# Kernel tuning notes

Measured on AMD Instinct MI355X. Metric: run time of the kernel, lower is better.

Reference implementation:

```python
import jax, jax.numpy as jnp
import numpy as np

B, N, E = 4, 10000, 160000
F_EXOG = 8
IN_DIM = 9          # 1 (pm25) + F_EXOG
HIST, PRED = 8, 12
HID = 64
GNN_OUT = 13
E_HID, E_OUT = 32, 30
GRU_IN = IN_DIM + GNN_OUT  # 22


def setup_inputs() -> dict:
    key = jax.random.key(0)
    ks = jax.random.split(key, 16)
    s = 0.1
    return {
        "pm25_hist": jax.random.normal(ks[0], (B, HIST, N, 1), jnp.float32),
        "feature": jax.random.normal(ks[1], (B, HIST + PRED, N, F_EXOG), jnp.float32),
        "edge_attr": jax.random.uniform(ks[2], (E, 2), jnp.float32),
        "wind_mean": jnp.array([2.0, 180.0], jnp.float32),
        "wind_std": jnp.array([1.5, 90.0], jnp.float32),
        # edge MLP: Linear(21->32), Sigmoid, Linear(32->30), Sigmoid
        "e_w1": jax.random.normal(ks[3], (2 * IN_DIM + 3, E_HID), jnp.float32) * s,
        "e_b1": jnp.zeros((E_HID,), jnp.float32),
        "e_w2": jax.random.normal(ks[4], (E_HID, E_OUT), jnp.float32) * s,
        "e_b2": jnp.zeros((E_OUT,), jnp.float32),
        # node MLP: Linear(30->13), Sigmoid
        "n_w": jax.random.normal(ks[5], (E_OUT, GNN_OUT), jnp.float32) * s,
        "n_b": jnp.zeros((GNN_OUT,), jnp.float32),
        # GRUCell(22 -> 64), torch layout: weight_ih (3H, in), weight_hh (3H, H)
        "gru_wi": jax.random.normal(ks[6], (3 * HID, GRU_IN), jnp.float32) * s,
        "gru_wh": jax.random.normal(ks[7], (3 * HID, HID), jnp.float32) * s,
        "gru_bi": jnp.zeros((3 * HID,), jnp.float32),
        "gru_bh": jnp.zeros((3 * HID,), jnp.float32),
        # fc_out: Linear(64 -> 1)
        "fc_w": jax.random.normal(ks[8], (HID, 1), jnp.float32) * s,
        "fc_b": jnp.zeros((1,), jnp.float32),
        "edge_index": jax.random.randint(ks[9], (2, E), 0, N, jnp.int64),
    }


def _forward(pm25_hist, feature, edge_attr, wind_mean, wind_std,
             e_w1, e_b1, e_w2, e_b2, n_w, n_b,
             gru_wi, gru_wh, gru_bi, gru_bh, fc_w, fc_b, edge_index):
    batch, _, n_nodes, _ = pm25_hist.shape
    src, tgt = edge_index[0], edge_index[1]

    # buffers precomputed in __init__ (torch.std uses ddof=1)
    edge_mean = edge_attr.mean(axis=0, keepdims=True)
    edge_std = jnp.maximum(jnp.std(edge_attr, axis=0, ddof=1, keepdims=True), 1e-6)
    edge_attr_norm = (edge_attr - edge_mean) / edge_std          # (E, 2)
    city_dist = jnp.maximum(edge_attr[:, 0], 1e-3)               # (E,)
    city_direc = edge_attr[:, 1]                                 # (E,)
    w_std = jnp.maximum(wind_std, 1e-6)

    def graph_gnn(x):                                            # x: (B, N, IN_DIM)
        node_src = x[:, src]                                     # (B, E, IN_DIM)
        node_tgt = x[:, tgt]
        wind = node_src[..., -2:] * w_std + wind_mean            # de-normalize
        speed = jnp.maximum(wind[..., 0], 0.0)                   # (B, E)
        wdir = jnp.deg2rad(wind[..., 1])
        theta = jnp.abs(city_direc - wdir)
        edge_w = jax.nn.relu(3.0 * speed * jnp.cos(theta) / city_dist)  # (B, E)
        ean = jnp.broadcast_to(edge_attr_norm, (x.shape[0], E, 2))
        h = jnp.concatenate([node_src, node_tgt, ean, edge_w[..., None]], axis=-1)
        h = jax.nn.sigmoid(h @ e_w1 + e_b1)
        h = jax.nn.sigmoid(h @ e_w2 + e_b2)                      # (B, E, E_OUT)
        agg = jnp.zeros((x.shape[0], n_nodes, E_OUT), x.dtype)
        agg = agg.at[:, tgt].add(h).at[:, src].add(-h)           # scatter add / sub
        return jax.nn.sigmoid(agg @ n_w + n_b)                   # (B, N, GNN_OUT)

    def gru_step(h, x):                                          # h,x: (B*N, .)
        gi = x @ gru_wi.T + gru_bi
        gh = h @ gru_wh.T + gru_bh
        i_r, i_z, i_n = jnp.split(gi, 3, axis=-1)
        h_r, h_z, h_n = jnp.split(gh, 3, axis=-1)
        r = jax.nn.sigmoid(i_r + h_r)
        z = jax.nn.sigmoid(i_z + h_z)
        n = jnp.tanh(i_n + r * h_n)
        return (1.0 - z) * n + z * h

    def step(carry, feat_t):
        hn, xn = carry                                           # (B*N,HID), (B,N,1)
        x = jnp.concatenate([xn, feat_t], axis=-1)               # (B, N, IN_DIM)
        x_gnn = graph_gnn(x)
        xc = jnp.concatenate([x_gnn, x], axis=-1).reshape(batch * n_nodes, -1)
        hn = gru_step(hn, xc)
        xn = hn.reshape(batch, n_nodes, HID) @ fc_w + fc_b       # (B, N, 1)
        return (hn, xn), xn[..., 0]

    hn0 = jnp.zeros((batch * n_nodes, HID), pm25_hist.dtype)
    xn0 = pm25_hist[:, -1]                                       # (B, N, 1)
    feats = jnp.swapaxes(feature[:, HIST:HIST + PRED], 0, 1)     # (PRED, B, N, F)
    _, preds = jax.lax.scan(step, (hn0, xn0), feats)             # (PRED, B, N)
    return jnp.transpose(preds, (1, 2, 0))                       # (B, N, PRED)


def reference(pm25_hist, feature, edge_attr, wind_mean, wind_std,
              e_w1, e_b1, e_w2, e_b2, n_w, n_b,
              gru_wi, gru_wh, gru_bi, gru_bh, fc_w, fc_b, edge_index):
    return _forward(pm25_hist, feature, edge_attr, wind_mean, wind_std,
                    e_w1, e_b1, e_w2, e_b2, n_w, n_b,
                    gru_wi, gru_wh, gru_bi, gru_bh, fc_w, fc_b, edge_index)
```

## Files before the change

kernel.cpp:

```cpp
#include <hip/hip_runtime.h>
#include <hip/hip_fp16.h>
#include <cstddef>

#define BB    4
#define NN    10000
#define EE    160000
#define BN    40000
#define HISTC 8
#define PREDC 12
#define TSTEP 20
#define FEX   8
#define HIDC  64
#define EHID  32
#define EOUTC 30
#define GOUTC 13
#define GINC  22

typedef float v2f __attribute__((ext_vector_type(2)));
typedef _Float16 v2h __attribute__((ext_vector_type(2)));

struct alignas(16) WPack {
    __half2 w[16];
    float   nw[14];
    float   b2;
    float   pad;
};

__device__ __forceinline__ float fast_rcp(float x) { return __builtin_amdgcn_rcpf(x); }
__device__ __forceinline__ float sigm(float x) {
    return fast_rcp(1.0f + __expf(-x));
}
__device__ __forceinline__ v2f sigm2(v2f x) {
    v2f r; r.x = sigm(x.x); r.y = sigm(x.y); return r;
}
__device__ __forceinline__ float tanh_fast(float x) {
    x = fminf(fmaxf(x, -15.0f), 15.0f);
    float e = __expf(2.0f * x);
    return (e - 1.0f) * fast_rcp(e + 1.0f);
}

__device__ __forceinline__ float dot2(__half2 a, __half2 b, float c) {
#if __has_builtin(__builtin_amdgcn_fdot2)
    union { __half2 h; v2h v; } ua, ub;
    ua.h = a; ub.h = b;
    return __builtin_amdgcn_fdot2(ua.v, ub.v, c, false);
#else
    float2 fa = __half22float2(a), fb = __half22float2(b);
    return c + fa.x * fb.x + fa.y * fb.y;
#endif
}

__global__ __launch_bounds__(256) void stats1_kernel(const float* __restrict__ ea,
                                                     double* __restrict__ part) {
    __shared__ double sm[256][4];
    int tid = threadIdx.x;
    double s0 = 0, s1 = 0, q0 = 0, q1 = 0;
    for (int e = blockIdx.x * 256 + tid; e < EE; e += 256 * 256) {
        float2 v = reinterpret_cast<const float2*>(ea)[e];
        double v0 = (double)v.x, v1 = (double)v.y;
        s0 += v0; q0 += v0 * v0;
        s1 += v1; q1 += v1 * v1;
    }
    sm[tid][0] = s0; sm[tid][1] = s1; sm[tid][2] = q0; sm[tid][3] = q1;
    __syncthreads();
    for (int off = 128; off > 0; off >>= 1) {
        if (tid < off)
            for (int k = 0; k < 4; k++) sm[tid][k] += sm[tid + off][k];
        __syncthreads();
    }
    if (tid == 0) {
        part[blockIdx.x * 4 + 0] = sm[0][0];
        part[blockIdx.x * 4 + 1] = sm[0][1];
        part[blockIdx.x * 4 + 2] = sm[0][2];
        part[blockIdx.x * 4 + 3] = sm[0][3];
    }
}

__global__ __launch_bounds__(256) void stats2_kernel(const double* __restrict__ part,
                                                     float* __restrict__ stats) {
    __shared__ double sm[256][4];
    int tid = threadIdx.x;
    sm[tid][0] = part[tid * 4 + 0];
    sm[tid][1] = part[tid * 4 + 1];
    sm[tid][2] = part[tid * 4 + 2];
    sm[tid][3] = part[tid * 4 + 3];
    __syncthreads();
    for (int off = 128; off > 0; off >>= 1) {
        if (tid < off)
            for (int k = 0; k < 4; k++) sm[tid][k] += sm[tid + off][k];
        __syncthreads();
    }
    if (tid == 0) {
        double m0 = sm[0][0] / EE, m1 = sm[0][1] / EE;
        double v0 = (sm[0][2] - sm[0][0] * sm[0][0] / EE) / (double)(EE - 1);
        double v1 = (sm[0][3] - sm[0][1] * sm[0][1] / EE) / (double)(EE - 1);
        float sd0 = fmaxf((float)sqrt(v0 > 0 ? v0 : 0.0), 1e-6f);
        float sd1 = fmaxf((float)sqrt(v1 > 0 ? v1 : 0.0), 1e-6f);
        stats[0] = (float)m0; stats[1] = (float)m1;
        stats[2] = 1.0f / sd0; stats[3] = 1.0f / sd1;
    }
}

__global__ __launch_bounds__(256) void edgepre_kernel(
    const float* __restrict__ ea, const float* __restrict__ stats,
    float4* __restrict__ epre4)
{
    int e = blockIdx.x * 256 + threadIdx.x;
    if (e >= EE) return;
    float2 v = reinterpret_cast<const float2*>(ea)[e];
    float4 r;
    r.x = (v.x - stats[0]) * stats[2];
    r.y = (v.y - stats[1]) * stats[3];
    r.z = 1.0f / fmaxf(v.x, 1e-3f);
    r.w = v.y;
    epre4[e] = r;
}

__global__ __launch_bounds__(256) void cvtw_kernel(
    const float* __restrict__ wi, const float* __restrict__ wh,
    const float* __restrict__ ew2, const float* __restrict__ eb2,
    const float* __restrict__ nw,
    __half* __restrict__ wi_h, __half* __restrict__ wh_h,
    WPack* __restrict__ wpack)
{
    int i = blockIdx.x * 256 + threadIdx.x;
    if (i < 192 * GINC) wi_h[i] = __float2half(wi[i]);
    if (i < 192 * HIDC) wh_h[i] = __float2half(wh[i]);
    if (i < EOUTC) {
        WPack wp;
        #pragma unroll
        for (int q = 0; q < 16; q++)
            wp.w[q] = __floats2half2_rn(ew2[(2 * q) * EOUTC + i],
                                        ew2[(2 * q + 1) * EOUTC + i]);
        #pragma unroll
        for (int j = 0; j < GOUTC; j++) wp.nw[j] = nw[i * GOUTC + j];
        wp.nw[13] = 0.f;
        wp.b2 = eb2[i];
        wp.pad = 0.f;
        wpack[i] = wp;
    }
}

__global__ void initxn_kernel(const float* __restrict__ pm, float* __restrict__ xn) {
    int i = blockIdx.x * 256 + threadIdx.x;
    if (i >= BN) return;
    int b = i / NN, n = i - b * NN;
    xn[i] = pm[(b * HISTC + (HISTC - 1)) * NN + n];
}

__global__ void hist_kernel(const int* __restrict__ eidx,
                            int* __restrict__ deg_t, int* __restrict__ deg_s) {
    int e = blockIdx.x * 256 + threadIdx.x;
    if (e >= EE) return;
    atomicAdd(&deg_s[eidx[e]], 1);
    atomicAdd(&deg_t[eidx[EE + e]], 1);
}

__global__ __launch_bounds__(1024) void scan_kernel(
    const int* __restrict__ deg_t, const int* __restrict__ deg_s,
    int* __restrict__ off_t, int* __restrict__ off_s,
    int* __restrict__ cnt_t, int* __restrict__ cnt_s)
{
    __shared__ int pt[1024], ps[1024];
    int tid = threadIdx.x;
    int base = tid * 10;
    int st = 0, ss = 0;
    for (int k = 0; k < 10; k++) {
        int i = base + k;
        if (i < NN) { st += deg_t[i]; ss += deg_s[i]; }
    }
    pt[tid] = st; ps[tid] = ss;
    __syncthreads();
    for (int off = 1; off < 1024; off <<= 1) {
        int vt = (tid >= off) ? pt[tid - off] : 0;
        int vs = (tid >= off) ? ps[tid - off] : 0;
        __syncthreads();
        pt[tid] += vt; ps[tid] += vs;
        __syncthreads();
    }
    int ext = (tid == 0) ? 0 : pt[tid - 1];
    int exs = (tid == 0) ? 0 : ps[tid - 1];
    for (int k = 0; k < 10; k++) {
        int i = base + k;
        if (i < NN) {
            off_t[i] = ext; cnt_t[i] = ext;
            off_s[i] = exs; cnt_s[i] = exs;
            ext += deg_t[i]; exs += deg_s[i];
        }
    }
    if (tid == 0) { off_t[NN] = EE; off_s[NN] = EE; }
}

__global__ void fill_kernel(const int* __restrict__ eidx,
                            int* __restrict__ cnt_t, int* __restrict__ cnt_s,
                            int4* __restrict__ epos)
{
    int e = blockIdx.x * 256 + threadIdx.x;
    if (e >= EE) return;
    int s = eidx[e];
    int g = eidx[EE + e];
    int pt = atomicAdd(&cnt_t[g], 1);
    int ps = atomicAdd(&cnt_s[s], 1);
    int4 r; r.x = s; r.y = g; r.z = pt; r.w = ps;
    epos[e] = r;
}

__global__ void perm_kernel(const int4* __restrict__ epos,
                            const float4* __restrict__ epre4,
                            int4* __restrict__ eT, float4* __restrict__ epreT)
{
    int e = blockIdx.x * 256 + threadIdx.x;
    if (e >= EE) return;
    int4 p = epos[e];
    int slot = p.z;
    int4 r; r.x = p.x; r.y = p.y; r.z = p.w; r.w = 0;
    eT[slot] = r;
    epreT[slot] = epre4[e];
}

__global__ __launch_bounds__(256) void pre_kernel(
    float* __restrict__ xncur, const float* __restrict__ feature, int t,
    const float* __restrict__ xp,
    const float* __restrict__ fb,
    const float* __restrict__ ew1,
    const float* __restrict__ wmean, const float* __restrict__ wstd,
    __half* __restrict__ preS, __half* __restrict__ preT,
    float2* __restrict__ wind2, float* __restrict__ out)
{
    __shared__ alignas(16) float w1s[18 * EHID];
    for (int i = threadIdx.x; i < 18 * EHID; i += 256) w1s[i] = ew1[i];
    __syncthreads();
    int idx = blockIdx.x * 256 + threadIdx.x;
    if (idx >= BN * 8) return;
    int i = idx >> 3;
    int c = idx & 7;
    int b = i / NN, n = i - b * NN;
    float x0;
    if (t == 0) {
        x0 = xncur[i];
    } else {
        x0 = (xp[i] + xp[BN + i]) + (xp[2 * BN + i] + xp[3 * BN + i]) + fb[0];
        if (c == 0) {
            xncur[i] = x0;
            out[(size_t)i * PREDC + (t - 1)] = x0;
        }
    }
    float x[9];
    x[0] = x0;
    {
        const float4* fp = reinterpret_cast<const float4*>(
            feature + (((size_t)b * TSTEP + HISTC + t) * NN + n) * FEX);
        float4 u = fp[0], v = fp[1];
        x[1] = u.x; x[2] = u.y; x[3] = u.z; x[4] = u.w;
        x[5] = v.x; x[6] = v.y; x[7] = v.z; x[8] = v.w;
    }
    float4 aS = {0.f, 0.f, 0.f, 0.f}, aT = {0.f, 0.f, 0.f, 0.f};
    #pragma unroll
    for (int k = 0; k < 9; k++) {
        float4 wS = reinterpret_cast<const float4*>(&w1s[k * EHID])[c];
        float4 wT = reinterpret_cast<const float4*>(&w1s[(9 + k) * EHID])[c];
        aS.x += x[k] * wS.x; aS.y += x[k] * wS.y; aS.z += x[k] * wS.z; aS.w += x[k] * wS.w;
        aT.x += x[k] * wT.x; aT.y += x[k] * wT.y; aT.z += x[k] * wT.z; aT.w += x[k] * wT.w;
    }
    union { uint2 u; __half h[4]; } sv, tv;
    sv.h[0] = __float2half(aS.x); sv.h[1] = __float2half(aS.y);
    sv.h[2] = __float2half(aS.z); sv.h[3] = __float2half(aS.w);
    tv.h[0] = __float2half(aT.x); tv.h[1] = __float2half(aT.y);
    tv.h[2] = __float2half(aT.z); tv.h[3] = __float2half(aT.w);
    reinterpret_cast<uint2*>(preS + (size_t)i * EHID)[c] = sv.u;
    reinterpret_cast<uint2*>(preT + (size_t)i * EHID)[c] = tv.u;
    if (c == 1) {
        float sd0 = fmaxf(wstd[0], 1e-6f), sd1 = fmaxf(wstd[1], 1e-6f);
        float speed = fmaxf(x[7] * sd0 + wmean[0], 0.f);
        float wdir  = (x[8] * sd1 + wmean[1]) * 0.017453292519943295f;
        float2 wv; wv.x = 3.0f * speed; wv.y = wdir;
        wind2[i] = wv;
    }
}

__global__ __launch_bounds__(256) void finalout_kernel(
    const float* __restrict__ xp, const float* __restrict__ fb,
    float* __restrict__ out)
{
    int i = blockIdx.x * 256 + threadIdx.x;
    if (i >= BN) return;
    out[(size_t)i * PREDC + (PREDC - 1)] =
        (xp[i] + xp[BN + i]) + (xp[2 * BN + i] + xp[3 * BN + i]) + fb[0];
}

__global__ __launch_bounds__(256) void edge_kernel(
    const int4* __restrict__ eT, const float4* __restrict__ epreT,
    const __half* __restrict__ preS, const __half* __restrict__ preT,
    const float2* __restrict__ wind2,
    const float* __restrict__ ew1, const float* __restrict__ eb1,
    const WPack* __restrict__ wpack,
    __half* __restrict__ h3t, __half* __restrict__ h3s)
{
    int i = blockIdx.x * 256 + threadIdx.x;
    int bA = blockIdx.y;
    int bB = bA + 2;
    int4 et = eT[i];
    int s = et.x, g = et.y, ps = et.z;
    float4 ep = epreT[i];

    size_t iSA = (size_t)bA * NN + s, iTA = (size_t)bA * NN + g;
    size_t iSB = (size_t)bB * NN + s, iTB = (size_t)bB * NN + g;
    float2 wA = wind2[iSA];
    float2 wB = wind2[iSB];
    v2f ew;
    ew.x = fmaxf(wA.x * __cosf(fabsf(ep.w - wA.y)) * ep.z, 0.f);
    ew.y = fmaxf(wB.x * __cosf(fabsf(ep.w - wB.y)) * ep.z, 0.f);

    union alignas(16) { uint4 u[4]; __half2 h2[16]; } RSA, RTA, RSB, RTB;
    {
        const uint4* p;
        p = reinterpret_cast<const uint4*>(preS + iSA * EHID);
        RSA.u[0] = p[0]; RSA.u[1] = p[1]; RSA.u[2] = p[2]; RSA.u[3] = p[3];
        p = reinterpret_cast<const uint4*>(preT + iTA * EHID);
        RTA.u[0] = p[0]; RTA.u[1] = p[1]; RTA.u[2] = p[2]; RTA.u[3] = p[3];
        p = reinterpret_cast<const uint4*>(preS + iSB * EHID);
        RSB.u[0] = p[0]; RSB.u[1] = p[1]; RSB.u[2] = p[2]; RSB.u[3] = p[3];
        p = reinterpret_cast<const uint4*>(preT + iTB * EHID);
        RTB.u[0] = p[0]; RTB.u[1] = p[1]; RTB.u[2] = p[2]; RTB.u[3] = p[3];
    }

    const v2f* W18 = reinterpret_cast<const v2f*>(ew1 + 18 * EHID);
    const v2f* W19 = reinterpret_cast<const v2f*>(ew1 + 19 * EHID);
    const v2f* W20 = reinterpret_cast<const v2f*>(ew1 + 20 * EHID);
    const v2f* B1  = reinterpret_cast<const v2f*>(eb1);
    float ean0 = ep.x, ean1 = ep.y;
    __half2 h1A[16], h1B[16];
    #pragma unroll
    for (int q = 0; q < 16; q++) {
        v2f base = W18[q] * ean0 + W19[q] * ean1 + B1[q];
        v2f w20q = W20[q];
        float2 rsA = __half22float2(RSA.h2[q]);
        float2 rtA = __half22float2(RTA.h2[q]);
        float2 rsB = __half22float2(RSB.h2[q]);
        float2 rtB = __half22float2(RTB.h2[q]);
        v2f uA, uB;
        uA.x = base.x + rsA.x + rtA.x + w20q.x * ew.x;
        uA.y = base.y + rsA.y + rtA.y + w20q.y * ew.x;
        uB.x = base.x + rsB.x + rtB.x + w20q.x * ew.y;
        uB.y = base.y + rsB.y + rtB.y + w20q.y * ew.y;
        v2f sA = sigm2(uA), sB = sigm2(uB);
        h1A[q] = __floats2half2_rn(sA.x, sA.y);
        h1B[q] = __floats2half2_rn(sB.x, sB.y);
    }

    v2f h3ab[GOUTC];
    #pragma unroll
    for (int j = 0; j < GOUTC; j++) { h3ab[j].x = 0.f; h3ab[j].y = 0.f; }
    for (int o = 0; o < EOUTC; o++) {
        const WPack* W = wpack + o;
        float accA0 = W->b2, accA1 = 0.f;
        float accB0 = W->b2, accB1 = 0.f;
        #pragma unroll
        for (int q = 0; q < 16; q += 2) {
            __half2 w0 = W->w[q], w1 = W->w[q + 1];
            accA0 = dot2(h1A[q],     w0, accA0);
            accB0 = dot2(h1B[q],     w0, accB0);
            accA1 = dot2(h1A[q + 1], w1, accA1);
            accB1 = dot2(h1B[q + 1], w1, accB1);
        }
        v2f h2ab; h2ab.x = sigm(accA0 + accA1); h2ab.y = sigm(accB0 + accB1);
        #pragma unroll
        for (int j = 0; j < GOUTC; j++) h3ab[j] += W->nw[j] * h2ab;
    }

    union alignas(16) { uint4 u[2]; __half h[16]; } rA, rB;
    #pragma unroll
    for (int j = 0; j < GOUTC; j++) {
        rA.h[j] = __float2half(h3ab[j].x);
        rB.h[j] = __float2half(h3ab[j].y);
    }
    #pragma unroll
    for (int j = GOUTC; j < 16; j++) { rA.h[j] = __float2half(0.f); rB.h[j] = __float2half(0.f); }
    {
        __half* oT = h3t + ((size_t)bA * EE + i) * 16;
        reinterpret_cast<uint4*>(oT)[0] = rA.u[0];
        reinterpret_cast<uint4*>(oT)[1] = rA.u[1];
        oT = h3t + ((size_t)bB * EE + i) * 16;
        reinterpret_cast<uint4*>(oT)[0] = rB.u[0];
        reinterpret_cast<uint4*>(oT)[1] = rB.u[1];
        __half* oS = h3s + ((size_t)bA * EE + ps) * 16;
        reinterpret_cast<uint4*>(oS)[0] = rA.u[0];
        reinterpret_cast<uint4*>(oS)[1] = rA.u[1];
        oS = h3s + ((size_t)bB * EE + ps) * 16;
        reinterpret_cast<uint4*>(oS)[0] = rB.u[0];
        reinterpret_cast<uint4*>(oS)[1] = rB.u[1];
    }
}

__global__ __launch_bounds__(256) void gather_kernel(
    const __half* __restrict__ h3t, const __half* __restrict__ h3s,
    const int* __restrict__ off_t, const int* __restrict__ off_s,
    float* __restrict__ agg)
{
    int n = (blockIdx.x * 256 + threadIdx.x) >> 6;
    if (n >= NN) return;
    n = __builtin_amdgcn_readfirstlane(n);
    int lane = threadIdx.x & 63;
    int b = lane >> 4, ch = lane & 15;
    const __half* ht = h3t + (size_t)b * EE * 16 + ch;
    const __half* hs = h3s + (size_t)b * EE * 16 + ch;
    float a0 = 0.f, a1 = 0.f, a2 = 0.f, a3 = 0.f;
    {
        int i0 = off_t[n], i1 = off_t[n + 1];
        int i = i0;
        for (; i + 4 <= i1; i += 4) {
            a0 += __half2float(ht[(size_t)(i + 0) * 16]);
            a1 += __half2float(ht[(size_t)(i + 1) * 16]);
            a2 += __half2float(ht[(size_t)(i + 2) * 16]);
            a3 += __half2float(ht[(size_t)(i + 3) * 16]);
        }
        for (; i < i1; i++) a0 += __half2float(ht[(size_t)i * 16]);
    }
    {
        int i0 = off_s[n], i1 = off_s[n + 1];
        int i = i0;
        for (; i + 4 <= i1; i += 4) {
            a0 -= __half2float(hs[(size_t)(i + 0) * 16]);
            a1 -= __half2float(hs[(size_t)(i + 1) * 16]);
            a2 -= __half2float(hs[(size_t)(i + 2) * 16]);
            a3 -= __half2float(hs[(size_t)(i + 3) * 16]);
        }
        for (; i < i1; i++) a0 -= __half2float(hs[(size_t)i * 16]);
    }
    agg[((size_t)b * NN + n) * 16 + ch] = (a0 + a1) + (a2 + a3);
}

__global__ __launch_bounds__(256) void node_kernel(
    const float* __restrict__ xncur, const float* __restrict__ feature, int t,
    const float* __restrict__ agg, const float* __restrict__ nb,
    const __half* __restrict__ wi_h, const __half* __restrict__ wh_h,
    const float* __restrict__ bi, const float* __restrict__ bh,
    const float* __restrict__ fw,
    const __half2* __restrict__ hnold, __half2* __restrict__ hnnew,
    float* __restrict__ xp)
{
    __shared__ float xpart[4][64];
    int lane = threadIdx.x & 63;
    int wav  = threadIdx.x >> 6;
    int jb   = blockIdx.y;
    int node = blockIdx.x * 64 + lane;
    int b = node / NN;
    int n = node - b * NN;

    float xc[GINC];
    {
        const float4* ar = reinterpret_cast<const float4*>(agg + (size_t)node * 16);
        float4 a0 = ar[0], a1 = ar[1], a2 = ar[2];
        float a3 = agg[(size_t)node * 16 + 12];
        xc[0] = sigm(a0.x + nb[0]);  xc[1] = sigm(a0.y + nb[1]);
        xc[2] = sigm(a0.z + nb[2]);  xc[3] = sigm(a0.w + nb[3]);
        xc[4] = sigm(a1.x + nb[4]);  xc[5] = sigm(a1.y + nb[5]);
        xc[6] = sigm(a1.z + nb[6]);  xc[7] = sigm(a1.w + nb[7]);
        xc[8] = sigm(a2.x + nb[8]);  xc[9] = sigm(a2.y + nb[9]);
        xc[10] = sigm(a2.z + nb[10]); xc[11] = sigm(a2.w + nb[11]);
        xc[12] = sigm(a3 + nb[12]);
    }
    xc[13] = xncur[node];
    {
        const float4* fp = reinterpret_cast<const float4*>(
            feature + (((size_t)b * TSTEP + HISTC + t) * NN + n) * FEX);
        float4 u = fp[0], v = fp[1];
        xc[14] = u.x; xc[15] = u.y; xc[16] = u.z; xc[17] = u.w;
        xc[18] = v.x; xc[19] = v.y; xc[20] = v.z; xc[21] = v.w;
    }
    __half2 xch[11];
    #pragma unroll
    for (int p = 0; p < 11; p++) xch[p] = __floats2half2_rn(xc[2*p], xc[2*p+1]);

    __half2 hh[32];
    #pragma unroll
    for (int p = 0; p < 32; p++) hh[p] = hnold[(size_t)p * BN + node];

    float xsum = 0.f;
    #pragma unroll
    for (int jj2 = 0; jj2 < 2; jj2++) {
        int j0 = __builtin_amdgcn_readfirstlane(jb * 16 + wav * 4 + jj2 * 2);
        union { __half2 h; __half v[2]; } holdw;
        holdw.h = hnold[(size_t)(j0 >> 1) * BN + node];
        float hnew2[2];
        #pragma unroll
        for (int d = 0; d < 2; d++) {
            int j = j0 + d;
            float ir = bi[j], iz = bi[64 + j], in_ = bi[128 + j];
            const __half2* wr0 = reinterpret_cast<const __half2*>(wi_h + (size_t)j * GINC);
            const __half2* wr1 = reinterpret_cast<const __half2*>(wi_h + (size_t)(64 + j) * GINC);
            const __half2* wr2 = reinterpret_cast<const __half2*>(wi_h + (size_t)(128 + j) * GINC);
            #pragma unroll
            for (int p = 0; p < 11; p++) {
                ir  = dot2(xch[p], wr0[p], ir);
                iz  = dot2(xch[p], wr1[p], iz);
                in_ = dot2(xch[p], wr2[p], in_);
            }
            float hr0 = bh[j], hz0 = bh[64 + j], hn0 = bh[128 + j];
            float hr1 = 0.f, hz1 = 0.f, hn1 = 0.f;
            const __half2* vr0 = reinterpret_cast<const __half2*>(wh_h + (size_t)j * HIDC);
            const __half2* vr1 = reinterpret_cast<const __half2*>(wh_h + (size_t)(64 + j) * HIDC);
            const __half2* vr2 = reinterpret_cast<const __half2*>(wh_h + (size_t)(128 + j) * HIDC);
            #pragma unroll
            for (int p = 0; p < 32; p += 2) {
                hr0 = dot2(hh[p],     vr0[p],     hr0);
                hz0 = dot2(hh[p],     vr1[p],     hz0);
                hn0 = dot2(hh[p],     vr2[p],     hn0);
                hr1 = dot2(hh[p + 1], vr0[p + 1], hr1);
                hz1 = dot2(hh[p + 1], vr1[p + 1], hz1);
                hn1 = dot2(hh[p + 1], vr2[p + 1], hn1);
            }
            float r  = sigm(ir + hr0 + hr1);
            float z  = sigm(iz + hz0 + hz1);
            float nn = tanh_fast(in_ + r * (hn0 + hn1));
            float hold = __half2float(holdw.v[d]);
            float hnew = (1.f - z) * nn + z * hold;
            hnew2[d] = hnew;
            xsum += hnew * fw[j];
        }
        hnnew[(size_t)(j0 >> 1) * BN + node] = __floats2half2_rn(hnew2[0], hnew2[1]);
    }
    xpart[wav][lane] = xsum;
    __syncthreads();
    if (wav == 0) {
        float tot = xpart[0][lane] + xpart[1][lane] + xpart[2][lane] + xpart[3][lane];
        xp[(size_t)jb * BN + node] = tot;
    }
}

extern "C" void kernel_launch(void* const* d_in, const int* in_sizes, int n_in,
                              void* d_out, int out_size, void* d_ws, size_t ws_size,
                              hipStream_t stream)
{
    const float* pm    = (const float*)d_in[0];
    const float* feat  = (const float*)d_in[1];
    const float* ea    = (const float*)d_in[2];
    const float* wmean = (const float*)d_in[3];
    const float* wstd  = (const float*)d_in[4];
    const float* ew1   = (const float*)d_in[5];
    const float* eb1   = (const float*)d_in[6];
    const float* ew2   = (const float*)d_in[7];
    const float* eb2   = (const float*)d_in[8];
    const float* nw    = (const float*)d_in[9];
    const float* nb    = (const float*)d_in[10];
    const float* wi    = (const float*)d_in[11];
    const float* wh    = (const float*)d_in[12];
    const float* bi    = (const float*)d_in[13];
    const float* bh    = (const float*)d_in[14];
    const float* fw    = (const float*)d_in[15];
    const float* fb    = (const float*)d_in[16];
    const int*   eidx  = (const int*)d_in[17];
    float* out = (float*)d_out;

    char* w = (char*)d_ws;
    double* partd = (double*)w;                    w += 256 * 4 * sizeof(double);
    float*  stats = (float*)w;                     w += 16 * sizeof(float);
    WPack*  wpack = (WPack*)w;                     w += EOUTC * sizeof(WPack);
    float4* epre4 = (float4*)w;                    w += (size_t)EE * sizeof(float4);
    float4* epreT = (float4*)w;                    w += (size_t)EE * sizeof(float4);
    float*  xncur = (float*)w;                     w += (size_t)BN * sizeof(float);
    float*  xp    = (float*)w;                     w += (size_t)4 * BN * sizeof(float);
    __half2* hnA  = (__half2*)w;                   w += (size_t)32 * BN * sizeof(__half2);
    __half2* hnB  = (__half2*)w;                   w += (size_t)32 * BN * sizeof(__half2);
    float*  agg13 = (float*)w;                     w += (size_t)BN * 16 * sizeof(float);
    __half* preS  = (__half*)w;                    w += (size_t)BN * EHID * sizeof(__half);
    __half* preT  = (__half*)w;                    w += (size_t)BN * EHID * sizeof(__half);
    float2* wind2 = (float2*)w;                    w += (size_t)BN * sizeof(float2);
    __half* h3t   = (__half*)w;                    w += (size_t)BB * EE * 16 * sizeof(__half);
    __half* h3s   = (__half*)w;                    w += (size_t)BB * EE * 16 * sizeof(__half);
    __half* wi_h  = (__half*)w;                    w += (size_t)192 * GINC * sizeof(__half);
    __half* wh_h  = (__half*)w;                    w += (size_t)192 * HIDC * sizeof(__half);
    int*    deg_t = (int*)w;                       w += NN * sizeof(int);
    int*    deg_s = (int*)w;                       w += NN * sizeof(int);
    int*    off_t = (int*)w;                       w += (NN + 1) * sizeof(int);
    int*    off_s = (int*)w;                       w += (NN + 1) * sizeof(int);
    int*    cnt_t = (int*)w;                       w += NN * sizeof(int);
    int*    cnt_s = (int*)w;                       w += NN * sizeof(int);
    int4*   epos  = (int4*)w;                      w += (size_t)EE * sizeof(int4);
    int4*   eT    = (int4*)w;                      w += (size_t)EE * sizeof(int4);

    stats1_kernel<<<256, 256, 0, stream>>>(ea, partd);
    stats2_kernel<<<1, 256, 0, stream>>>(partd, stats);
    edgepre_kernel<<<(EE + 255) / 256, 256, 0, stream>>>(ea, stats, epre4);
    cvtw_kernel<<<(192 * HIDC + 255) / 256, 256, 0, stream>>>(
        wi, wh, ew2, eb2, nw, wi_h, wh_h, wpack);
    initxn_kernel<<<(BN + 255) / 256, 256, 0, stream>>>(pm, xncur);
    hipMemsetAsync(hnA, 0, (size_t)32 * BN * sizeof(__half2), stream);
    hipMemsetAsync(deg_t, 0, 2 * NN * sizeof(int), stream);
    hist_kernel<<<(EE + 255) / 256, 256, 0, stream>>>(eidx, deg_t, deg_s);
    scan_kernel<<<1, 1024, 0, stream>>>(deg_t, deg_s, off_t, off_s, cnt_t, cnt_s);
    fill_kernel<<<(EE + 255) / 256, 256, 0, stream>>>(eidx, cnt_t, cnt_s, epos);
    perm_kernel<<<(EE + 255) / 256, 256, 0, stream>>>(epos, epre4, eT, epreT);

    for (int t = 0; t < PREDC; t++) {
        const __half2* hnold = (t & 1) ? hnB : hnA;
        __half2*       hnnew = (t & 1) ? hnA : hnB;
        pre_kernel<<<(BN * 8 + 255) / 256, 256, 0, stream>>>(
            xncur, feat, t, xp, fb, ew1, wmean, wstd, preS, preT, wind2, out);
        edge_kernel<<<dim3(EE / 256, 2), 256, 0, stream>>>(
            eT, epreT, preS, preT, wind2, ew1, eb1, wpack, h3t, h3s);
        gather_kernel<<<(NN * 64 + 255) / 256, 256, 0, stream>>>(
            h3t, h3s, off_t, off_s, agg13);
        node_kernel<<<dim3(BN / 64, 4), 256, 0, stream>>>(
            xncur, feat, t, agg13, nb, wi_h, wh_h, bi, bh, fw, hnold, hnnew, xp);
    }
    finalout_kernel<<<(BN + 255) / 256, 256, 0, stream>>>(xp, fb, out);
}
```

Before: 1.069 ms.

## Interleave per-batch edge outputs so gather reads contiguous 128-byte rows

Edge outputs h3t/h3s move from a batch-major layout [B][E][16] to an edge-major layout [E][B*16]. Each edge thread now handles adjacent batch pairs (0,1) or (2,3) and writes one 64-byte chunk per pair. In the gather kernel all 64 lanes (4 batches × 16 channels) then read one contiguous 128-byte row per edge instead of four scattered 32-byte segments. The aim is better coalescing of the gather, which runs every timestep, in exchange for a changed pairing of batches inside the edge kernel.

```diff
diff --git a/kernel.cpp b/kernel.cpp
--- a/kernel.cpp
+++ b/kernel.cpp
@@ -297,8 +297,8 @@
     __half* __restrict__ h3t, __half* __restrict__ h3s)
 {
     int i = blockIdx.x * 256 + threadIdx.x;
-    int bA = blockIdx.y;
-    int bB = bA + 2;
+    int bA = blockIdx.y * 2;
+    int bB = bA + 1;
     int4 et = eT[i];
     int s = et.x, g = et.y, ps = et.z;
     float4 ep = epreT[i];
@@ -368,27 +368,25 @@
         for (int j = 0; j < GOUTC; j++) h3ab[j] += W->nw[j] * h2ab;
     }
 
-    union alignas(16) { uint4 u[2]; __half h[16]; } rA, rB;
+    union alignas(16) { uint4 u[4]; __half h[32]; } r;
     #pragma unroll
     for (int j = 0; j < GOUTC; j++) {
-        rA.h[j] = __float2half(h3ab[j].x);
-        rB.h[j] = __float2half(h3ab[j].y);
-    }
-    #pragma unroll
-    for (int j = GOUTC; j < 16; j++) { rA.h[j] = __float2half(0.f); rB.h[j] = __float2half(0.f); }
+        r.h[j]      = __float2half(h3ab[j].x);
+        r.h[16 + j] = __float2half(h3ab[j].y);
+    }
+    #pragma unroll
+    for (int j = GOUTC; j < 16; j++) { r.h[j] = __float2half(0.f); r.h[16 + j] = __float2half(0.f); }
     {
-        __half* oT = h3t + ((size_t)bA * EE + i) * 16;
-        reinterpret_cast<uint4*>(oT)[0] = rA.u[0];
-        reinterpret_cast<uint4*>(oT)[1] = rA.u[1];
-        oT = h3t + ((size_t)bB * EE + i) * 16;
-        reinterpret_cast<uint4*>(oT)[0] = rB.u[0];
-        reinterpret_cast<uint4*>(oT)[1] = rB.u[1];
-        __half* oS = h3s + ((size_t)bA * EE + ps) * 16;
-        reinterpret_cast<uint4*>(oS)[0] = rA.u[0];
-        reinterpret_cast<uint4*>(oS)[1] = rA.u[1];
-        oS = h3s + ((size_t)bB * EE + ps) * 16;
-        reinterpret_cast<uint4*>(oS)[0] = rB.u[0];
-        reinterpret_cast<uint4*>(oS)[1] = rB.u[1];
+        __half* oT = h3t + (size_t)i * 64 + blockIdx.y * 32;
+        reinterpret_cast<uint4*>(oT)[0] = r.u[0];
+        reinterpret_cast<uint4*>(oT)[1] = r.u[1];
+        reinterpret_cast<uint4*>(oT)[2] = r.u[2];
+        reinterpret_cast<uint4*>(oT)[3] = r.u[3];
+        __half* oS = h3s + (size_t)ps * 64 + blockIdx.y * 32;
+        reinterpret_cast<uint4*>(oS)[0] = r.u[0];
+        reinterpret_cast<uint4*>(oS)[1] = r.u[1];
+        reinterpret_cast<uint4*>(oS)[2] = r.u[2];
+        reinterpret_cast<uint4*>(oS)[3] = r.u[3];
     }
 }
 
@@ -402,30 +400,30 @@
     n = __builtin_amdgcn_readfirstlane(n);
     int lane = threadIdx.x & 63;
     int b = lane >> 4, ch = lane & 15;
-    const __half* ht = h3t + (size_t)b * EE * 16 + ch;
-    const __half* hs = h3s + (size_t)b * EE * 16 + ch;
+    const __half* ht = h3t + lane;
+    const __half* hs = h3s + lane;
     float a0 = 0.f, a1 = 0.f, a2 = 0.f, a3 = 0.f;
     {
         int i0 = off_t[n], i1 = off_t[n + 1];
         int i = i0;
         for (; i + 4 <= i1; i += 4) {
-            a0 += __half2float(ht[(size_t)(i + 0) * 16]);
-            a1 += __half2float(ht[(size_t)(i + 1) * 16]);
-            a2 += __half2float(ht[(size_t)(i + 2) * 16]);
-            a3 += __half2float(ht[(size_t)(i + 3) * 16]);
+            a0 += __half2float(ht[(size_t)(i + 0) * 64]);
+            a1 += __half2float(ht[(size_t)(i + 1) * 64]);
+            a2 += __half2float(ht[(size_t)(i + 2) * 64]);
+            a3 += __half2float(ht[(size_t)(i + 3) * 64]);
         }
-        for (; i < i1; i++) a0 += __half2float(ht[(size_t)i * 16]);
+        for (; i < i1; i++) a0 += __half2float(ht[(size_t)i * 64]);
     }
     {
         int i0 = off_s[n], i1 = off_s[n + 1];
         int i = i0;
         for (; i + 4 <= i1; i += 4) {
-            a0 -= __half2float(hs[(size_t)(i + 0) * 16]);
-            a1 -= __half2float(hs[(size_t)(i + 1) * 16]);
-            a2 -= __half2float(hs[(size_t)(i + 2) * 16]);
-            a3 -= __half2float(hs[(size_t)(i + 3) * 16]);
+            a0 -= __half2float(hs[(size_t)(i + 0) * 64]);
+            a1 -= __half2float(hs[(size_t)(i + 1) * 64]);
+            a2 -= __half2float(hs[(size_t)(i + 2) * 64]);
+            a3 -= __half2float(hs[(size_t)(i + 3) * 64]);
         }
-        for (; i < i1; i++) a0 -= __half2float(hs[(size_t)i * 16]);
+        for (; i < i1; i++) a0 -= __half2float(hs[(size_t)i * 64]);
     }
     agg[((size_t)b * NN + n) * 16 + ch] = (a0 + a1) + (a2 + a3);
 }
@@ -566,8 +564,8 @@
     __half* preS  = (__half*)w;                    w += (size_t)BN * EHID * sizeof(__half);
     __half* preT  = (__half*)w;                    w += (size_t)BN * EHID * sizeof(__half);
     float2* wind2 = (float2*)w;                    w += (size_t)BN * sizeof(float2);
-    __half* h3t   = (__half*)w;                    w += (size_t)BB * EE * 16 * sizeof(__half);
-    __half* h3s   = (__half*)w;                    w += (size_t)BB * EE * 16 * sizeof(__half);
+    __half* h3t   = (__half*)w;                    w += (size_t)EE * 64 * sizeof(__half);
+    __half* h3s   = (__half*)w;                    w += (size_t)EE * 64 * sizeof(__half);
     __half* wi_h  = (__half*)w;                    w += (size_t)192 * GINC * sizeof(__half);
     __half* wh_h  = (__half*)w;                    w += (size_t)192 * HIDC * sizeof(__half);
     int*    deg_t = (int*)w;                       w += NN * sizeof(int);
```

Result: slower. 1.097 ms (+2.6%).
